# Optimization experiments

Measured on AMD Instinct MI355X. Metric: run time of the kernel, lower is better.

Reference implementation:

```python
import jax, jax.numpy as jnp
import numpy as np

B, S, DIM = 2, 2048, 1024
H, W = 16, 256
HD = DIM // H
SCALE = HD ** -0.5


def setup_inputs() -> dict:
    key = jax.random.key(0)
    ks = jax.random.split(key, 9)
    std = DIM ** -0.5
    return {
        "x": jax.random.normal(ks[0], (B, S, DIM), dtype=jnp.float32),
        "Wq": jax.random.normal(ks[1], (DIM, DIM), dtype=jnp.float32) * std,
        "bq": jnp.zeros((DIM,), dtype=jnp.float32),
        "Wk": jax.random.normal(ks[2], (DIM, DIM), dtype=jnp.float32) * std,
        "bk": jnp.zeros((DIM,), dtype=jnp.float32),
        "Wv": jax.random.normal(ks[3], (DIM, DIM), dtype=jnp.float32) * std,
        "bv": jnp.zeros((DIM,), dtype=jnp.float32),
        "Wo": jax.random.normal(ks[4], (DIM, DIM), dtype=jnp.float32) * std,
        "bo": jnp.zeros((DIM,), dtype=jnp.float32),
    }


def reference(x, Wq, bq, Wk, bk, Wv, bv, Wo, bo):
    b, s, dim = x.shape
    q = (x @ Wq + bq).reshape(b, s, H, HD).transpose(0, 2, 1, 3)  # [B,H,S,HD]
    k = (x @ Wk + bk).reshape(b, s, H, HD).transpose(0, 2, 1, 3)
    v = (x @ Wv + bv).reshape(b, s, H, HD).transpose(0, 2, 1, 3)

    scores = jnp.einsum("bhid,bhjd->bhij", q, k) * SCALE  # [B,H,S,S]
    i = jnp.arange(s)[:, None]
    j = jnp.arange(s)[None, :]
    # valid keys: within causal sliding window [i-W+1, i]
    valid = (j <= i) & (j >= i - W + 1)
    scores = jnp.where(valid, scores, -jnp.inf)
    attn = jax.nn.softmax(scores, axis=-1)
    out = jnp.einsum("bhij,bhjd->bhid", attn, v)  # [B,H,S,HD]
    out = out.transpose(0, 2, 1, 3).reshape(b, s, dim)
    return out @ Wo + bo
```

## Files before the change

### kernel.cpp

```cpp
#include <hip/hip_runtime.h>
#include <stdint.h>

typedef __bf16 bf16;
typedef __bf16 bf16x8 __attribute__((ext_vector_type(8)));
typedef float f32x4 __attribute__((ext_vector_type(4)));

#define MFMA16(a, b, c) __builtin_amdgcn_mfma_f32_16x16x32_bf16((a), (b), (c), 0, 0, 0)

__device__ __forceinline__ void ldsdma16(const void* g, void* l) {
  __builtin_amdgcn_global_load_lds((const __attribute__((address_space(1))) void*)g,
                                   (__attribute__((address_space(3))) void*)l, 16, 0, 0);
}

__global__ __launch_bounds__(256) void prep_cast(const float* __restrict__ x,
                                                 bf16* __restrict__ xb) {
  int idx = (blockIdx.x * 256 + threadIdx.x) * 4;
  float4 v = *(const float4*)(x + idx);
  union { bf16 h[4]; uint2 u; } p;
  p.h[0] = (bf16)v.x; p.h[1] = (bf16)v.y; p.h[2] = (bf16)v.z; p.h[3] = (bf16)v.w;
  *(uint2*)(xb + idx) = p.u;
}

__global__ __launch_bounds__(256) void prep_transpose(const float* __restrict__ Wq,
                                                      const float* __restrict__ Wk,
                                                      const float* __restrict__ Wv,
                                                      const float* __restrict__ Wo,
                                                      bf16* __restrict__ WT) {
  __shared__ float tile[64][65];
  const float* src = blockIdx.z == 0 ? Wq : blockIdx.z == 1 ? Wk : blockIdx.z == 2 ? Wv : Wo;
  bf16* dst = WT + (size_t)blockIdx.z * 1024 * 1024;
  const int k0 = blockIdx.y * 64, n0 = blockIdx.x * 64;
  const int rr = threadIdx.x >> 6, c = threadIdx.x & 63;
#pragma unroll
  for (int i = 0; i < 16; ++i) {
    int r = i * 4 + rr;
    tile[r][c] = src[(size_t)(k0 + r) * 1024 + n0 + c];
  }
  __syncthreads();
#pragma unroll
  for (int i = 0; i < 16; ++i) {
    int r = i * 4 + rr;
    dst[(size_t)(n0 + r) * 1024 + k0 + c] = (bf16)tile[c][r];
  }
}

__device__ __forceinline__ void gemm_mainloop(const bf16* __restrict__ A,
                                              const bf16* __restrict__ BT, int K,
                                              int m0, int n0, bf16* As, bf16* Bs,
                                              f32x4 acc[4][4]) {
  const int tid = threadIdx.x;
  const int lane = tid & 63;
  const int wave = tid >> 6;
  const int wm = wave >> 1, wn = wave & 1;
  const int quad = lane >> 4, l16 = lane & 15;

  const f32x4 zero = {0.f, 0.f, 0.f, 0.f};
#pragma unroll
  for (int i = 0; i < 4; ++i)
#pragma unroll
    for (int j = 0; j < 4; ++j) acc[i][j] = zero;

  const int ch0 = wave * 128 + lane;

  for (int k0 = 0; k0 < K; k0 += 32) {
#pragma unroll
    for (int c = 0; c < 2; ++c) {
      int chunk = ch0 + c * 64;
      int row = chunk >> 2;
      int cg = (chunk & 3) ^ ((row >> 1) & 3);
      ldsdma16(A + (size_t)(m0 + row) * K + k0 + cg * 8,
               (char*)As + (size_t)(wave * 128 + c * 64) * 16);
      ldsdma16(BT + (size_t)(n0 + row) * K + k0 + cg * 8,
               (char*)Bs + (size_t)(wave * 128 + c * 64) * 16);
    }
    __syncthreads();
    bf16x8 af[4], bfv[4];
#pragma unroll
    for (int i = 0; i < 4; ++i) {
      int ra = wm * 64 + i * 16 + l16;
      af[i] = ((const bf16x8*)As)[ra * 4 + (quad ^ ((ra >> 1) & 3))];
      int rb = wn * 64 + i * 16 + l16;
      bfv[i] = ((const bf16x8*)Bs)[rb * 4 + (quad ^ ((rb >> 1) & 3))];
    }
#pragma unroll
    for (int i = 0; i < 4; ++i)
#pragma unroll
      for (int j = 0; j < 4; ++j) acc[i][j] = MFMA16(af[i], bfv[j], acc[i][j]);
    __syncthreads();
  }
}

__global__ __launch_bounds__(256) void qkv_gemm(const bf16* __restrict__ xb,
                                                const bf16* __restrict__ WT,
                                                const float* __restrict__ bq,
                                                const float* __restrict__ bk,
                                                const float* __restrict__ bv,
                                                bf16* __restrict__ Qd,
                                                bf16* __restrict__ Kd,
                                                bf16* __restrict__ Vd) {
  __shared__ bf16 As[128 * 32] __attribute__((aligned(16)));
  __shared__ bf16 Bs[128 * 32] __attribute__((aligned(16)));
  f32x4 acc[4][4];
  const int m0 = blockIdx.y * 128, n0 = blockIdx.x * 128;
  gemm_mainloop(xb, WT, 1024, m0, n0, As, Bs, acc);

  const int lane = threadIdx.x & 63, wave = threadIdx.x >> 6;
  const int wm = wave >> 1, wn = wave & 1;
  const int quad = lane >> 4, l16 = lane & 15;
#pragma unroll
  for (int j = 0; j < 4; ++j) {
    const int n = n0 + wn * 64 + j * 16 + l16;
    const int sel = n >> 10, d = n & 1023;
    const float bias = (sel == 0 ? bq : sel == 1 ? bk : bv)[d];
    bf16* dst = (sel == 0 ? Qd : sel == 1 ? Kd : Vd);
    const float scl = (sel == 0) ? 0.125f : 1.f;
    const int h = d >> 6, hd = d & 63;
#pragma unroll
    for (int i = 0; i < 4; ++i) {
#pragma unroll
      for (int r = 0; r < 4; ++r) {
        const int token = m0 + wm * 64 + i * 16 + quad * 4 + r;
        const int bb = token >> 11, s = token & 2047;
        const float v = (acc[i][j][r] + bias) * scl;
        dst[((((size_t)bb * 16 + h) * 2048 + s) << 6) + hd] = (bf16)v;
      }
    }
  }
}

__global__ __launch_bounds__(256) void attn_kernel(const bf16* __restrict__ Q,
                                                   const bf16* __restrict__ K,
                                                   const bf16* __restrict__ V,
                                                   bf16* __restrict__ Ao) {
  __shared__ bf16 Qs[64 * 64] __attribute__((aligned(16)));
  __shared__ bf16 Ks[64 * 64] __attribute__((aligned(16)));
  __shared__ bf16 Vt[64 * 72] __attribute__((aligned(16)));
  __shared__ bf16 Ps[4][16 * 72] __attribute__((aligned(16)));

  const int tid = threadIdx.x, lane = tid & 63, wave = tid >> 6;
  const int quad = lane >> 4, l16 = lane & 15;
  const int qt = blockIdx.x, h = blockIdx.y, b = blockIdx.z;
  const int q0 = qt * 64;
  const size_t base = ((size_t)(b * 16 + h)) * 2048 * 64;
  const bf16* Qb = Q + base + (size_t)q0 * 64;
  const bf16* Kb = K + base;
  const bf16* Vb = V + base;

#pragma unroll
  for (int c = 0; c < 2; ++c) {
    int chunk = wave * 128 + c * 64 + lane;
    int row = chunk >> 3;
    int cg = (chunk & 7) ^ (row & 7);
    ldsdma16(Qb + (size_t)row * 64 + cg * 8, (char*)Qs + (size_t)(wave * 128 + c * 64) * 16);
  }
  __syncthreads();

  bf16x8 qa[2];
  {
    int row = wave * 16 + l16;
    qa[0] = ((const bf16x8*)Qs)[row * 8 + ((0 * 4 + quad) ^ (row & 7))];
    qa[1] = ((const bf16x8*)Qs)[row * 8 + ((1 * 4 + quad) ^ (row & 7))];
  }

  float mrow[4], lrow[4];
  f32x4 oacc[4];
  const f32x4 zero = {0.f, 0.f, 0.f, 0.f};
#pragma unroll
  for (int r = 0; r < 4; ++r) { mrow[r] = -1e30f; lrow[r] = 0.f; }
#pragma unroll
  for (int t = 0; t < 4; ++t) oacc[t] = zero;

  const int clo = (qt >= 4) ? (qt - 4) : 0;
  for (int ck = clo; ck <= qt; ++ck) {
    const int c0 = ck * 64;
    __syncthreads();
#pragma unroll
    for (int c = 0; c < 2; ++c) {
      int chunk = wave * 128 + c * 64 + lane;
      int row = chunk >> 3;
      int cg = (chunk & 7) ^ (row & 7);
      ldsdma16(Kb + (size_t)(c0 + row) * 64 + cg * 8,
               (char*)Ks + (size_t)(wave * 128 + c * 64) * 16);
    }
    {
      int key = tid >> 2, hc = (tid & 3) * 16;
      const bf16* vp = Vb + (size_t)(c0 + key) * 64 + hc;
      bf16x8 v0 = *(const bf16x8*)vp;
      bf16x8 v1 = *(const bf16x8*)(vp + 8);
#pragma unroll
      for (int i = 0; i < 8; ++i) Vt[(hc + i) * 72 + key] = v0[i];
#pragma unroll
      for (int i = 0; i < 8; ++i) Vt[(hc + 8 + i) * 72 + key] = v1[i];
    }
    __syncthreads();

    f32x4 sc[4];
#pragma unroll
    for (int nt = 0; nt < 4; ++nt) {
      int key = nt * 16 + l16;
      bf16x8 kb0 = ((const bf16x8*)Ks)[key * 8 + ((0 * 4 + quad) ^ (key & 7))];
      bf16x8 kb1 = ((const bf16x8*)Ks)[key * 8 + ((1 * 4 + quad) ^ (key & 7))];
      f32x4 s = zero;
      s = MFMA16(qa[0], kb0, s);
      s = MFMA16(qa[1], kb1, s);
      sc[nt] = s;
    }

    float alpha[4];
#pragma unroll
    for (int r = 0; r < 4; ++r) {
      const int i = q0 + wave * 16 + quad * 4 + r;
      float mx = -1e30f;
#pragma unroll
      for (int nt = 0; nt < 4; ++nt) {
        const int j = c0 + nt * 16 + l16;
        const bool valid = (j <= i) && (j + 255 >= i);
        const float s = valid ? sc[nt][r] : -1e30f;
        sc[nt][r] = s;
        mx = fmaxf(mx, s);
      }
#pragma unroll
      for (int m = 8; m >= 1; m >>= 1) mx = fmaxf(mx, __shfl_xor(mx, m, 64));
      const float mnew = fmaxf(mrow[r], mx);
      alpha[r] = __expf(mrow[r] - mnew);
      mrow[r] = mnew;
      float rs = 0.f;
#pragma unroll
      for (int nt = 0; nt < 4; ++nt) {
        const float p = __expf(sc[nt][r] - mnew);
        sc[nt][r] = p;
        rs += p;
      }
#pragma unroll
      for (int m = 8; m >= 1; m >>= 1) rs += __shfl_xor(rs, m, 64);
      lrow[r] = lrow[r] * alpha[r] + rs;
    }

#pragma unroll
    for (int nt = 0; nt < 4; ++nt)
#pragma unroll
      for (int r = 0; r < 4; ++r)
        Ps[wave][(quad * 4 + r) * 72 + nt * 16 + l16] = (bf16)sc[nt][r];
    asm volatile("s_waitcnt lgkmcnt(0)" ::: "memory");
    bf16x8 pa0 = ((const bf16x8*)Ps[wave])[l16 * 9 + quad];
    bf16x8 pa1 = ((const bf16x8*)Ps[wave])[l16 * 9 + 4 + quad];

#pragma unroll
    for (int ht = 0; ht < 4; ++ht) {
      f32x4 o = oacc[ht];
#pragma unroll
      for (int r = 0; r < 4; ++r) o[r] *= alpha[r];
      const int n = ht * 16 + l16;
      bf16x8 vb0 = ((const bf16x8*)Vt)[n * 9 + quad];
      bf16x8 vb1 = ((const bf16x8*)Vt)[n * 9 + 4 + quad];
      o = MFMA16(pa0, vb0, o);
      o = MFMA16(pa1, vb1, o);
      oacc[ht] = o;
    }
  }

#pragma unroll
  for (int r = 0; r < 4; ++r) {
    const float inv = 1.f / lrow[r];
    const int row = q0 + wave * 16 + quad * 4 + r;
    const size_t outb = ((size_t)(b * 2048 + row)) * 1024 + h * 64;
#pragma unroll
    for (int ht = 0; ht < 4; ++ht)
      Ao[outb + ht * 16 + l16] = (bf16)(oacc[ht][r] * inv);
  }
}

__global__ __launch_bounds__(256) void out_gemm(const bf16* __restrict__ Ain,
                                                const bf16* __restrict__ WoT,
                                                const float* __restrict__ bo,
                                                float* __restrict__ out) {
  __shared__ bf16 As[128 * 32] __attribute__((aligned(16)));
  __shared__ bf16 Bs[128 * 32] __attribute__((aligned(16)));
  f32x4 acc[4][4];
  const int m0 = blockIdx.y * 128, n0 = blockIdx.x * 128;
  gemm_mainloop(Ain, WoT, 1024, m0, n0, As, Bs, acc);

  const int lane = threadIdx.x & 63, wave = threadIdx.x >> 6;
  const int wm = wave >> 1, wn = wave & 1;
  const int quad = lane >> 4, l16 = lane & 15;
#pragma unroll
  for (int j = 0; j < 4; ++j) {
    const int n = n0 + wn * 64 + j * 16 + l16;
    const float bias = bo[n];
#pragma unroll
    for (int i = 0; i < 4; ++i) {
#pragma unroll
      for (int r = 0; r < 4; ++r) {
        const int token = m0 + wm * 64 + i * 16 + quad * 4 + r;
        out[(size_t)token * 1024 + n] = acc[i][j][r] + bias;
      }
    }
  }
}

extern "C" void kernel_launch(void* const* d_in, const int* in_sizes, int n_in,
                              void* d_out, int out_size, void* d_ws, size_t ws_size,
                              hipStream_t stream) {
  const float* x  = (const float*)d_in[0];
  const float* Wq = (const float*)d_in[1];
  const float* bq = (const float*)d_in[2];
  const float* Wk = (const float*)d_in[3];
  const float* bk = (const float*)d_in[4];
  const float* Wv = (const float*)d_in[5];
  const float* bv = (const float*)d_in[6];
  const float* Wo = (const float*)d_in[7];
  const float* bo = (const float*)d_in[8];
  float* out = (float*)d_out;

  char* ws = (char*)d_ws;
  bf16* xb = (bf16*)(ws);
  bf16* WT = (bf16*)(ws + ((size_t)8 << 20));
  bf16* Qd = (bf16*)(ws + ((size_t)16 << 20));
  bf16* Kd = (bf16*)(ws + ((size_t)24 << 20));
  bf16* Vd = (bf16*)(ws + ((size_t)32 << 20));
  bf16* Ao = (bf16*)(ws + ((size_t)40 << 20));

  prep_cast<<<4096, 256, 0, stream>>>(x, xb);
  prep_transpose<<<dim3(16, 16, 4), 256, 0, stream>>>(Wq, Wk, Wv, Wo, WT);
  qkv_gemm<<<dim3(24, 32), 256, 0, stream>>>(xb, WT, bq, bk, bv, Qd, Kd, Vd);
  attn_kernel<<<dim3(32, 16, 2), 256, 0, stream>>>(Qd, Kd, Vd, Ao);
  out_gemm<<<dim3(8, 32), 256, 0, stream>>>(Ao, WT + (size_t)3 * 1024 * 1024, bo, out);
}
```

Before: 174.4 us.

## Merge prep kernels, use 128-key attention chunks, and halve out_gemm N tile

Merges the input cast and weight transpose into one prep launch, with an extra z-slice that handles the cast. The attention kernel now runs the sliding window as up to three phases: a masked 128-key lower-edge chunk, an unmasked 128-key chunk and a causal diagonal 64-key chunk. This replaces per-element masking over five 64-key chunks and loads Q straight into registers, with MFMA priority hints added. out_gemm switches to 128x64 tiles so it launches twice as many blocks and fills the device better. The trade-offs are larger LDS use per attention block and more template code paths.

```diff
diff --git a/kernel.cpp b/kernel.cpp
--- a/kernel.cpp
+++ b/kernel.cpp
@@ -12,21 +12,26 @@
                                    (__attribute__((address_space(3))) void*)l, 16, 0, 0);
 }
 
-__global__ __launch_bounds__(256) void prep_cast(const float* __restrict__ x,
-                                                 bf16* __restrict__ xb) {
-  int idx = (blockIdx.x * 256 + threadIdx.x) * 4;
-  float4 v = *(const float4*)(x + idx);
-  union { bf16 h[4]; uint2 u; } p;
-  p.h[0] = (bf16)v.x; p.h[1] = (bf16)v.y; p.h[2] = (bf16)v.z; p.h[3] = (bf16)v.w;
-  *(uint2*)(xb + idx) = p.u;
-}
-
-__global__ __launch_bounds__(256) void prep_transpose(const float* __restrict__ Wq,
-                                                      const float* __restrict__ Wk,
-                                                      const float* __restrict__ Wv,
-                                                      const float* __restrict__ Wo,
-                                                      bf16* __restrict__ WT) {
+__global__ __launch_bounds__(256) void prep_kernel(const float* __restrict__ x,
+                                                   const float* __restrict__ Wq,
+                                                   const float* __restrict__ Wk,
+                                                   const float* __restrict__ Wv,
+                                                   const float* __restrict__ Wo,
+                                                   bf16* __restrict__ xb,
+                                                   bf16* __restrict__ WT) {
   __shared__ float tile[64][65];
+  if (blockIdx.z == 4) {
+    const int t = (blockIdx.y * 16 + blockIdx.x) * 256 + threadIdx.x;
+#pragma unroll
+    for (int i = 0; i < 16; ++i) {
+      const int idx = (t + i * 65536) * 4;
+      float4 v = *(const float4*)(x + idx);
+      union { bf16 h[4]; uint2 u; } p;
+      p.h[0] = (bf16)v.x; p.h[1] = (bf16)v.y; p.h[2] = (bf16)v.z; p.h[3] = (bf16)v.w;
+      *(uint2*)(xb + idx) = p.u;
+    }
+    return;
+  }
   const float* src = blockIdx.z == 0 ? Wq : blockIdx.z == 1 ? Wk : blockIdx.z == 2 ? Wv : Wo;
   bf16* dst = WT + (size_t)blockIdx.z * 1024 * 1024;
   const int k0 = blockIdx.y * 64, n0 = blockIdx.x * 64;
@@ -44,10 +49,12 @@
   }
 }
 
+template <int NJ>
 __device__ __forceinline__ void gemm_mainloop(const bf16* __restrict__ A,
                                               const bf16* __restrict__ BT, int K,
                                               int m0, int n0, bf16* As, bf16* Bs,
-                                              f32x4 acc[4][4]) {
+                                              f32x4 (&acc)[4][NJ]) {
+  constexpr int BN = NJ * 32;
   const int tid = threadIdx.x;
   const int lane = tid & 63;
   const int wave = tid >> 6;
@@ -58,34 +65,41 @@
 #pragma unroll
   for (int i = 0; i < 4; ++i)
 #pragma unroll
-    for (int j = 0; j < 4; ++j) acc[i][j] = zero;
-
-  const int ch0 = wave * 128 + lane;
+    for (int j = 0; j < NJ; ++j) acc[i][j] = zero;
 
   for (int k0 = 0; k0 < K; k0 += 32) {
 #pragma unroll
     for (int c = 0; c < 2; ++c) {
-      int chunk = ch0 + c * 64;
+      int chunk = wave * 128 + c * 64 + lane;
       int row = chunk >> 2;
       int cg = (chunk & 3) ^ ((row >> 1) & 3);
       ldsdma16(A + (size_t)(m0 + row) * K + k0 + cg * 8,
                (char*)As + (size_t)(wave * 128 + c * 64) * 16);
+    }
+#pragma unroll
+    for (int c = 0; c < BN / 64; ++c) {
+      int chunk = wave * (BN / 64) * 64 + c * 64 + lane;
+      int row = chunk >> 2;
+      int cg = (chunk & 3) ^ ((row >> 1) & 3);
       ldsdma16(BT + (size_t)(n0 + row) * K + k0 + cg * 8,
-               (char*)Bs + (size_t)(wave * 128 + c * 64) * 16);
+               (char*)Bs + (size_t)(wave * (BN / 64) * 64 + c * 64) * 16);
     }
     __syncthreads();
-    bf16x8 af[4], bfv[4];
+    bf16x8 af[4], bfv[NJ];
 #pragma unroll
     for (int i = 0; i < 4; ++i) {
       int ra = wm * 64 + i * 16 + l16;
       af[i] = ((const bf16x8*)As)[ra * 4 + (quad ^ ((ra >> 1) & 3))];
-      int rb = wn * 64 + i * 16 + l16;
-      bfv[i] = ((const bf16x8*)Bs)[rb * 4 + (quad ^ ((rb >> 1) & 3))];
+    }
+#pragma unroll
+    for (int j = 0; j < NJ; ++j) {
+      int rb = wn * (BN / 2) + j * 16 + l16;
+      bfv[j] = ((const bf16x8*)Bs)[rb * 4 + (quad ^ ((rb >> 1) & 3))];
     }
 #pragma unroll
     for (int i = 0; i < 4; ++i)
 #pragma unroll
-      for (int j = 0; j < 4; ++j) acc[i][j] = MFMA16(af[i], bfv[j], acc[i][j]);
+      for (int j = 0; j < NJ; ++j) acc[i][j] = MFMA16(af[i], bfv[j], acc[i][j]);
     __syncthreads();
   }
 }
@@ -102,7 +116,7 @@
   __shared__ bf16 Bs[128 * 32] __attribute__((aligned(16)));
   f32x4 acc[4][4];
   const int m0 = blockIdx.y * 128, n0 = blockIdx.x * 128;
-  gemm_mainloop(xb, WT, 1024, m0, n0, As, Bs, acc);
+  gemm_mainloop<4>(xb, WT, 1024, m0, n0, As, Bs, acc);
 
   const int lane = threadIdx.x & 63, wave = threadIdx.x >> 6;
   const int wm = wave >> 1, wn = wave & 1;
@@ -128,14 +142,133 @@
   }
 }
 
+template <int NT, int MODE>
+__device__ __forceinline__ void attn_phase(const int start, const bf16* __restrict__ Kb,
+                                           const bf16* __restrict__ Vb, bf16* Ks, bf16* Vt,
+                                           bf16* Psw, const bf16x8 qa0, const bf16x8 qa1,
+                                           const int i0, float (&mrow)[4], float (&lrow)[4],
+                                           f32x4 (&oacc)[4]) {
+  const int tid = threadIdx.x, lane = tid & 63, wave = tid >> 6;
+  const int quad = lane >> 4, l16 = lane & 15;
+  const f32x4 zero = {0.f, 0.f, 0.f, 0.f};
+
+  __syncthreads();
+#pragma unroll
+  for (int c = 0; c < NT / 2; ++c) {
+    int chunk = c * 256 + wave * 64 + lane;
+    int row = chunk >> 3;
+    int cg = (chunk & 7) ^ (row & 7);
+    ldsdma16(Kb + (size_t)(start + row) * 64 + cg * 8,
+             (char*)Ks + (size_t)(c * 256 + wave * 64) * 16);
+  }
+  if (NT == 8) {
+    const int key = tid >> 1, hc = (tid & 1) * 32;
+    const bf16* vp = Vb + (size_t)(start + key) * 64 + hc;
+    bf16x8 v0 = ((const bf16x8*)vp)[0], v1 = ((const bf16x8*)vp)[1];
+    bf16x8 v2 = ((const bf16x8*)vp)[2], v3 = ((const bf16x8*)vp)[3];
+#pragma unroll
+    for (int i = 0; i < 8; ++i) Vt[(hc + i) * 136 + key] = v0[i];
+#pragma unroll
+    for (int i = 0; i < 8; ++i) Vt[(hc + 8 + i) * 136 + key] = v1[i];
+#pragma unroll
+    for (int i = 0; i < 8; ++i) Vt[(hc + 16 + i) * 136 + key] = v2[i];
+#pragma unroll
+    for (int i = 0; i < 8; ++i) Vt[(hc + 24 + i) * 136 + key] = v3[i];
+  } else {
+    const int key = tid >> 2, hc = (tid & 3) * 16;
+    const bf16* vp = Vb + (size_t)(start + key) * 64 + hc;
+    bf16x8 v0 = ((const bf16x8*)vp)[0], v1 = ((const bf16x8*)vp)[1];
+#pragma unroll
+    for (int i = 0; i < 8; ++i) Vt[(hc + i) * 136 + key] = v0[i];
+#pragma unroll
+    for (int i = 0; i < 8; ++i) Vt[(hc + 8 + i) * 136 + key] = v1[i];
+  }
+  __syncthreads();
+
+  f32x4 sc[NT];
+  __builtin_amdgcn_s_setprio(1);
+#pragma unroll
+  for (int nt = 0; nt < NT; ++nt) {
+    int key = nt * 16 + l16;
+    bf16x8 kb0 = ((const bf16x8*)Ks)[key * 8 + ((0 * 4 + quad) ^ (key & 7))];
+    bf16x8 kb1 = ((const bf16x8*)Ks)[key * 8 + ((1 * 4 + quad) ^ (key & 7))];
+    f32x4 s = zero;
+    s = MFMA16(qa0, kb0, s);
+    s = MFMA16(qa1, kb1, s);
+    sc[nt] = s;
+  }
+  __builtin_amdgcn_s_setprio(0);
+
+  float alpha[4];
+#pragma unroll
+  for (int r = 0; r < 4; ++r) {
+    const int i = i0 + r;
+    float mx = -1e30f;
+#pragma unroll
+    for (int nt = 0; nt < NT; ++nt) {
+      float s = sc[nt][r];
+      if (MODE == 1) {
+        const bool valid = (start + nt * 16 + l16 + 255 >= i);
+        s = valid ? s : -1e30f;
+        sc[nt][r] = s;
+      } else if (MODE == 2) {
+        const bool valid = (start + nt * 16 + l16 <= i);
+        s = valid ? s : -1e30f;
+        sc[nt][r] = s;
+      }
+      mx = fmaxf(mx, s);
+    }
+#pragma unroll
+    for (int m = 8; m >= 1; m >>= 1) mx = fmaxf(mx, __shfl_xor(mx, m, 64));
+    const float mnew = fmaxf(mrow[r], mx);
+    alpha[r] = __expf(mrow[r] - mnew);
+    mrow[r] = mnew;
+    float rs = 0.f;
+#pragma unroll
+    for (int nt = 0; nt < NT; ++nt) {
+      const float p = __expf(sc[nt][r] - mnew);
+      sc[nt][r] = p;
+      rs += p;
+    }
+#pragma unroll
+    for (int m = 8; m >= 1; m >>= 1) rs += __shfl_xor(rs, m, 64);
+    lrow[r] = lrow[r] * alpha[r] + rs;
+  }
+
+#pragma unroll
+  for (int nt = 0; nt < NT; ++nt)
+#pragma unroll
+    for (int r = 0; r < 4; ++r)
+      Psw[(quad * 4 + r) * 136 + nt * 16 + l16] = (bf16)sc[nt][r];
+  asm volatile("s_waitcnt lgkmcnt(0)" ::: "memory");
+  bf16x8 pa[NT / 2];
+#pragma unroll
+  for (int ks = 0; ks < NT / 2; ++ks)
+    pa[ks] = ((const bf16x8*)Psw)[l16 * 17 + ks * 4 + quad];
+
+  __builtin_amdgcn_s_setprio(1);
+#pragma unroll
+  for (int ht = 0; ht < 4; ++ht) {
+    f32x4 o = oacc[ht];
+#pragma unroll
+    for (int r = 0; r < 4; ++r) o[r] *= alpha[r];
+#pragma unroll
+    for (int ks = 0; ks < NT / 2; ++ks) {
+      bf16x8 vb = ((const bf16x8*)Vt)[(ht * 16 + l16) * 17 + ks * 4 + quad];
+      o = MFMA16(pa[ks], vb, o);
+    }
+    oacc[ht] = o;
+  }
+  __builtin_amdgcn_s_setprio(0);
+}
+
 __global__ __launch_bounds__(256) void attn_kernel(const bf16* __restrict__ Q,
                                                    const bf16* __restrict__ K,
                                                    const bf16* __restrict__ V,
                                                    bf16* __restrict__ Ao) {
-  __shared__ bf16 Qs[64 * 64] __attribute__((aligned(16)));
-  __shared__ bf16 Ks[64 * 64] __attribute__((aligned(16)));
-  __shared__ bf16 Vt[64 * 72] __attribute__((aligned(16)));
-  __shared__ bf16 Ps[4][16 * 72] __attribute__((aligned(16)));
+  __shared__ bf16 Ks[128 * 64] __attribute__((aligned(16)));
+  __shared__ bf16 Vt[64 * 136] __attribute__((aligned(16)));
+  __shared__ bf16 Ps[4][16 * 136] __attribute__((aligned(16)));
 
   const int tid = threadIdx.x, lane = tid & 63, wave = tid >> 6;
   const int quad = lane >> 4, l16 = lane & 15;
@@ -146,21 +279,9 @@
   const bf16* Kb = K + base;
   const bf16* Vb = V + base;
 
-#pragma unroll
-  for (int c = 0; c < 2; ++c) {
-    int chunk = wave * 128 + c * 64 + lane;
-    int row = chunk >> 3;
-    int cg = (chunk & 7) ^ (row & 7);
-    ldsdma16(Qb + (size_t)row * 64 + cg * 8, (char*)Qs + (size_t)(wave * 128 + c * 64) * 16);
-  }
-  __syncthreads();
-
-  bf16x8 qa[2];
-  {
-    int row = wave * 16 + l16;
-    qa[0] = ((const bf16x8*)Qs)[row * 8 + ((0 * 4 + quad) ^ (row & 7))];
-    qa[1] = ((const bf16x8*)Qs)[row * 8 + ((1 * 4 + quad) ^ (row & 7))];
-  }
+  const bf16* qrow = Qb + (size_t)(wave * 16 + l16) * 64 + quad * 8;
+  const bf16x8 qa0 = *(const bf16x8*)qrow;
+  const bf16x8 qa1 = *(const bf16x8*)(qrow + 32);
 
   float mrow[4], lrow[4];
   f32x4 oacc[4];
@@ -170,94 +291,18 @@
 #pragma unroll
   for (int t = 0; t < 4; ++t) oacc[t] = zero;
 
-  const int clo = (qt >= 4) ? (qt - 4) : 0;
-  for (int ck = clo; ck <= qt; ++ck) {
-    const int c0 = ck * 64;
-    __syncthreads();
-#pragma unroll
-    for (int c = 0; c < 2; ++c) {
-      int chunk = wave * 128 + c * 64 + lane;
-      int row = chunk >> 3;
-      int cg = (chunk & 7) ^ (row & 7);
-      ldsdma16(Kb + (size_t)(c0 + row) * 64 + cg * 8,
-               (char*)Ks + (size_t)(wave * 128 + c * 64) * 16);
-    }
-    {
-      int key = tid >> 2, hc = (tid & 3) * 16;
-      const bf16* vp = Vb + (size_t)(c0 + key) * 64 + hc;
-      bf16x8 v0 = *(const bf16x8*)vp;
-      bf16x8 v1 = *(const bf16x8*)(vp + 8);
-#pragma unroll
-      for (int i = 0; i < 8; ++i) Vt[(hc + i) * 72 + key] = v0[i];
-#pragma unroll
-      for (int i = 0; i < 8; ++i) Vt[(hc + 8 + i) * 72 + key] = v1[i];
-    }
-    __syncthreads();
-
-    f32x4 sc[4];
-#pragma unroll
-    for (int nt = 0; nt < 4; ++nt) {
-      int key = nt * 16 + l16;
-      bf16x8 kb0 = ((const bf16x8*)Ks)[key * 8 + ((0 * 4 + quad) ^ (key & 7))];
-      bf16x8 kb1 = ((const bf16x8*)Ks)[key * 8 + ((1 * 4 + quad) ^ (key & 7))];
-      f32x4 s = zero;
-      s = MFMA16(qa[0], kb0, s);
-      s = MFMA16(qa[1], kb1, s);
-      sc[nt] = s;
-    }
-
-    float alpha[4];
-#pragma unroll
-    for (int r = 0; r < 4; ++r) {
-      const int i = q0 + wave * 16 + quad * 4 + r;
-      float mx = -1e30f;
-#pragma unroll
-      for (int nt = 0; nt < 4; ++nt) {
-        const int j = c0 + nt * 16 + l16;
-        const bool valid = (j <= i) && (j + 255 >= i);
-        const float s = valid ? sc[nt][r] : -1e30f;
-        sc[nt][r] = s;
-        mx = fmaxf(mx, s);
-      }
-#pragma unroll
-      for (int m = 8; m >= 1; m >>= 1) mx = fmaxf(mx, __shfl_xor(mx, m, 64));
-      const float mnew = fmaxf(mrow[r], mx);
-      alpha[r] = __expf(mrow[r] - mnew);
-      mrow[r] = mnew;
-      float rs = 0.f;
-#pragma unroll
-      for (int nt = 0; nt < 4; ++nt) {
-        const float p = __expf(sc[nt][r] - mnew);
-        sc[nt][r] = p;
-        rs += p;
-      }
-#pragma unroll
-      for (int m = 8; m >= 1; m >>= 1) rs += __shfl_xor(rs, m, 64);
-      lrow[r] = lrow[r] * alpha[r] + rs;
-    }
-
-#pragma unroll
-    for (int nt = 0; nt < 4; ++nt)
-#pragma unroll
-      for (int r = 0; r < 4; ++r)
-        Ps[wave][(quad * 4 + r) * 72 + nt * 16 + l16] = (bf16)sc[nt][r];
-    asm volatile("s_waitcnt lgkmcnt(0)" ::: "memory");
-    bf16x8 pa0 = ((const bf16x8*)Ps[wave])[l16 * 9 + quad];
-    bf16x8 pa1 = ((const bf16x8*)Ps[wave])[l16 * 9 + 4 + quad];
-
-#pragma unroll
-    for (int ht = 0; ht < 4; ++ht) {
-      f32x4 o = oacc[ht];
-#pragma unroll
-      for (int r = 0; r < 4; ++r) o[r] *= alpha[r];
-      const int n = ht * 16 + l16;
-      bf16x8 vb0 = ((const bf16x8*)Vt)[n * 9 + quad];
-      bf16x8 vb1 = ((const bf16x8*)Vt)[n * 9 + 4 + quad];
-      o = MFMA16(pa0, vb0, o);
-      o = MFMA16(pa1, vb1, o);
-      oacc[ht] = o;
-    }
-  }
+  const int i0 = q0 + wave * 16 + quad * 4;
+  bf16* Psw = Ps[wave];
+
+  if (q0 >= 256)
+    attn_phase<8, 1>(q0 - 256, Kb, Vb, Ks, Vt, Psw, qa0, qa1, i0, mrow, lrow, oacc);
+  else if (q0 == 192)
+    attn_phase<4, 0>(0, Kb, Vb, Ks, Vt, Psw, qa0, qa1, i0, mrow, lrow, oacc);
+  if (q0 >= 128)
+    attn_phase<8, 0>(q0 - 128, Kb, Vb, Ks, Vt, Psw, qa0, qa1, i0, mrow, lrow, oacc);
+  else if (q0 == 64)
+    attn_phase<4, 0>(0, Kb, Vb, Ks, Vt, Psw, qa0, qa1, i0, mrow, lrow, oacc);
+  attn_phase<4, 2>(q0, Kb, Vb, Ks, Vt, Psw, qa0, qa1, i0, mrow, lrow, oacc);
 
 #pragma unroll
   for (int r = 0; r < 4; ++r) {
@@ -275,17 +320,17 @@
                                                 const float* __restrict__ bo,
                                                 float* __restrict__ out) {
   __shared__ bf16 As[128 * 32] __attribute__((aligned(16)));
-  __shared__ bf16 Bs[128 * 32] __attribute__((aligned(16)));
-  f32x4 acc[4][4];
-  const int m0 = blockIdx.y * 128, n0 = blockIdx.x * 128;
-  gemm_mainloop(Ain, WoT, 1024, m0, n0, As, Bs, acc);
+  __shared__ bf16 Bs[64 * 32] __attribute__((aligned(16)));
+  f32x4 acc[4][2];
+  const int m0 = blockIdx.y * 128, n0 = blockIdx.x * 64;
+  gemm_mainloop<2>(Ain, WoT, 1024, m0, n0, As, Bs, acc);
 
   const int lane = threadIdx.x & 63, wave = threadIdx.x >> 6;
   const int wm = wave >> 1, wn = wave & 1;
   const int quad = lane >> 4, l16 = lane & 15;
 #pragma unroll
-  for (int j = 0; j < 4; ++j) {
-    const int n = n0 + wn * 64 + j * 16 + l16;
+  for (int j = 0; j < 2; ++j) {
+    const int n = n0 + wn * 32 + j * 16 + l16;
     const float bias = bo[n];
 #pragma unroll
     for (int i = 0; i < 4; ++i) {
@@ -320,9 +365,8 @@
   bf16* Vd = (bf16*)(ws + ((size_t)32 << 20));
   bf16* Ao = (bf16*)(ws + ((size_t)40 << 20));
 
-  prep_cast<<<4096, 256, 0, stream>>>(x, xb);
-  prep_transpose<<<dim3(16, 16, 4), 256, 0, stream>>>(Wq, Wk, Wv, Wo, WT);
+  prep_kernel<<<dim3(16, 16, 5), 256, 0, stream>>>(x, Wq, Wk, Wv, Wo, xb, WT);
   qkv_gemm<<<dim3(24, 32), 256, 0, stream>>>(xb, WT, bq, bk, bv, Qd, Kd, Vd);
   attn_kernel<<<dim3(32, 16, 2), 256, 0, stream>>>(Qd, Kd, Vd, Ao);
-  out_gemm<<<dim3(8, 32), 256, 0, stream>>>(Ao, WT + (size_t)3 * 1024 * 1024, bo, out);
-}
+  out_gemm<<<dim3(16, 32), 256, 0, stream>>>(Ao, WT + (size_t)3 * 1024 * 1024, bo, out);
+}
```

Measured after the change: 168.3 us. -3.5%, faster.
